# Performance work log

Hardware: AMD Instinct MI355X
Metric: run time of the kernel (lower is better)

Reference implementation:

```python
import jax, jax.numpy as jnp
import numpy as np

B, R, F = 64, 196, 2048   # batch, regions, feature_dim
E, H, A = 512, 512, 512   # embed_dim, hidden_dim, attn_dim
V, L = 12000, 24          # vocab, seq_len


def setup_inputs() -> dict:
    key = jax.random.key(0)
    ks = jax.random.split(key, 16)
    s = lambda *d: 1.0 / np.sqrt(d[-1])
    inp = {
        'image_feats': jax.random.normal(ks[0], (B, R, F), jnp.float32),
        'caption_in': jax.random.randint(ks[1], (B, L), 0, V, jnp.int64),
        'emb_table': jax.random.normal(ks[2], (V, E), jnp.float32) * 0.02,
        'W_init_h': jax.random.normal(ks[3], (H, F), jnp.float32) * s(F),
        'b_init_h': jnp.zeros((H,), jnp.float32),
        'W_init_c': jax.random.normal(ks[4], (H, F), jnp.float32) * s(F),
        'b_init_c': jnp.zeros((H,), jnp.float32),
        'W_ih': jax.random.normal(ks[5], (4 * H, E + F), jnp.float32) * s(E + F),
        'b_ih': jnp.zeros((4 * H,), jnp.float32),
        'W_hh': jax.random.normal(ks[6], (4 * H, H), jnp.float32) * s(H),
        'b_hh': jnp.zeros((4 * H,), jnp.float32),
        'W_featp': jax.random.normal(ks[7], (A, F), jnp.float32) * s(F),
        'b_featp': jnp.zeros((A,), jnp.float32),
        'W_hidp': jax.random.normal(ks[8], (A, H), jnp.float32) * s(H),
        'b_hidp': jnp.zeros((A,), jnp.float32),
        'W_score': jax.random.normal(ks[9], (1, A), jnp.float32) * s(A),
        'b_score': jnp.zeros((1,), jnp.float32),
        'W_out': jax.random.normal(ks[10], (V, H), jnp.float32) * s(H),
        'b_out': jnp.zeros((V,), jnp.float32),
    }
    return inp


def _forward(image_feats, caption_in, emb_table, W_init_h, b_init_h, W_init_c,
             b_init_c, W_ih, b_ih, W_hh, b_hh, W_featp, b_featp, W_hidp,
             b_hidp, W_score, b_score, W_out, b_out):
    # init hidden state from mean image features
    mean_feats = image_feats.mean(axis=1)                      # (B, F)
    h0 = mean_feats @ W_init_h.T + b_init_h                    # (B, H)
    c0 = mean_feats @ W_init_c.T + b_init_c                    # (B, H)

    embeddings = emb_table[caption_in]                         # (B, L, E)  (dropout in eval mode = identity)

    # feature projection is constant over timesteps -> hoist out of the scan
    feat_proj = jnp.einsum('brf,af->bra', image_feats, W_featp) + b_featp  # (B, R, A)

    def step(carry, emb_t):
        h, c = carry
        # additive attention
        hid_proj = h @ W_hidp.T + b_hidp                       # (B, A)
        energy = jnp.tanh(feat_proj + hid_proj[:, None, :])    # (B, R, A)
        scores = jnp.einsum('bra,a->br', energy, W_score[0]) + b_score[0]
        alpha = jax.nn.softmax(scores, axis=1)                 # (B, R)
        context = jnp.einsum('br,brf->bf', alpha, image_feats) # (B, F)
        # LSTM cell (PyTorch gate order: i, f, g, o)
        x = jnp.concatenate([emb_t, context], axis=1)          # (B, E+F)
        gates = x @ W_ih.T + b_ih + h @ W_hh.T + b_hh          # (B, 4H)
        i, f, g, o = jnp.split(gates, 4, axis=1)
        c_new = jax.nn.sigmoid(f) * c + jax.nn.sigmoid(i) * jnp.tanh(g)
        h_new = jax.nn.sigmoid(o) * jnp.tanh(c_new)
        out = h_new @ W_out.T + b_out                          # (B, V)
        return (h_new, c_new), (out, alpha)

    emb_t = jnp.swapaxes(embeddings, 0, 1)                     # (L, B, E)
    _, (preds, alphas) = jax.lax.scan(step, (h0, c0), emb_t)
    predictions = jnp.swapaxes(preds, 0, 1)                    # (B, L, V)
    all_alphas = jnp.swapaxes(alphas, 0, 1)                    # (B, L, R)
    return predictions, all_alphas


def reference(image_feats, caption_in, emb_table, W_init_h, b_init_h, W_init_c,
              b_init_c, W_ih, b_ih, W_hh, b_hh, W_featp, b_featp, W_hidp,
              b_hidp, W_score, b_score, W_out, b_out):
    return _forward(image_feats, caption_in, emb_table, W_init_h, b_init_h,
                    W_init_c, b_init_c, W_ih, b_ih, W_hh, b_hh, W_featp,
                    b_featp, W_hidp, b_hidp, W_score, b_score, W_out, b_out)
```

## Files before the change

kernel.cpp:

```cpp
#include <hip/hip_runtime.h>

#define B_ 64
#define R_ 196
#define F_ 2048
#define E_ 512
#define H_ 512
#define A_ 512
#define V_ 12000
#define L_ 24

typedef __attribute__((ext_vector_type(8))) short bf16x8;
typedef __attribute__((ext_vector_type(8))) unsigned short ushort8_t;
typedef __attribute__((ext_vector_type(4))) float f32x4;
typedef unsigned short ush;

__device__ __forceinline__ float fast_tanh(float x) {
    float t = __expf(2.f * x);
    return 1.f - 2.f / (t + 1.f);
}
__device__ __forceinline__ float fast_sig(float x) {
    return 1.f / (1.f + __expf(-x));
}
__device__ __forceinline__ ush f2bf(float x) {
    unsigned int u = __float_as_uint(x);
    return (ush)((u + 0x7fffu + ((u >> 16) & 1u)) >> 16);
}
__device__ __forceinline__ float bf2f(ush b) {
    return __uint_as_float(((unsigned int)b) << 16);
}

#define LROW 40

template<int SPLIT, int CMAP, bool NFAST>
__global__ __launch_bounds__(256) void gemm_big(
    const ush* __restrict__ Ah, const ush* __restrict__ Al, int lda,
    const ush* __restrict__ Wh, const ush* __restrict__ Wl, int ldw,
    const float* __restrict__ bias, void* __restrict__ Cv,
    int ldc, int N, int K)
{
    constexpr int SMEM_BYTES = (SPLIT == 3) ? 51200 : 25600;
    __shared__ __align__(16) char smem[SMEM_BYTES];
    ush* sAh = (ush*)smem;
    ush* sBh = (ush*)(smem + 5120);
    ush* sAl = (ush*)(smem + 25600);
    ush* sBl = (ush*)(smem + 30720);

    const int tid = threadIdx.x;
    const int lane = tid & 63, w = tid >> 6;

    const int nbx = gridDim.x, nby = gridDim.y;
    const int nwg = nbx * nby;
    int lin = blockIdx.x + nbx * blockIdx.y;
    if ((nwg & 7) == 0) {
        const int q = nwg >> 3;
        lin = (lin & 7) * q + (lin >> 3);
    }
    int bx, by;
    if constexpr (NFAST) { by = lin % nby; bx = lin / nby; }
    else                 { bx = lin % nbx; by = lin / nbx; }
    const int mtile = bx * 64;
    const int ntile = by * 256;

    const int fr = lane & 15, kg = (lane >> 4) * 8;
    const int arow = tid >> 2, aq = (tid & 3) * 8;

    f32x4 acc[4][4];
    #pragma unroll
    for (int mf = 0; mf < 4; ++mf)
        #pragma unroll
        for (int nf = 0; nf < 4; ++nf) acc[mf][nf] = {0.f, 0.f, 0.f, 0.f};

    const uint4 zv = make_uint4(0u, 0u, 0u, 0u);

    for (int kb = 0; kb < K; kb += 32) {
        uint4 a_h = *(const uint4*)(Ah + (size_t)(mtile + arow) * lda + kb + aq);
        uint4 a_l;
        uint4 b_h[4], b_l[4];
        #pragma unroll
        for (int p = 0; p < 4; ++p) {
            const int row = ntile + arow + 64 * p;
            b_h[p] = (row < N) ? *(const uint4*)(Wh + (size_t)row * ldw + kb + aq) : zv;
        }
        if constexpr (SPLIT == 3) {
            a_l = *(const uint4*)(Al + (size_t)(mtile + arow) * lda + kb + aq);
            #pragma unroll
            for (int p = 0; p < 4; ++p) {
                const int row = ntile + arow + 64 * p;
                b_l[p] = (row < N) ? *(const uint4*)(Wl + (size_t)row * ldw + kb + aq) : zv;
            }
        }

        __syncthreads();
        *(uint4*)(sAh + arow * LROW + aq) = a_h;
        #pragma unroll
        for (int p = 0; p < 4; ++p)
            *(uint4*)(sBh + (arow + 64 * p) * LROW + aq) = b_h[p];
        if constexpr (SPLIT == 3) {
            *(uint4*)(sAl + arow * LROW + aq) = a_l;
            #pragma unroll
            for (int p = 0; p < 4; ++p)
                *(uint4*)(sBl + (arow + 64 * p) * LROW + aq) = b_l[p];
        }
        __syncthreads();

        bf16x8 bh[4], bl[4];
        #pragma unroll
        for (int nf = 0; nf < 4; ++nf) {
            bh[nf] = *(const bf16x8*)(sBh + (w * 64 + nf * 16 + fr) * LROW + kg);
            if constexpr (SPLIT == 3)
                bl[nf] = *(const bf16x8*)(sBl + (w * 64 + nf * 16 + fr) * LROW + kg);
        }
        #pragma unroll
        for (int mf = 0; mf < 4; ++mf) {
            const bf16x8 ah = *(const bf16x8*)(sAh + (mf * 16 + fr) * LROW + kg);
            if constexpr (SPLIT == 3) {
                const bf16x8 al = *(const bf16x8*)(sAl + (mf * 16 + fr) * LROW + kg);
                #pragma unroll
                for (int nf = 0; nf < 4; ++nf) {
                    acc[mf][nf] = __builtin_amdgcn_mfma_f32_16x16x32_bf16(ah, bh[nf], acc[mf][nf], 0, 0, 0);
                    acc[mf][nf] = __builtin_amdgcn_mfma_f32_16x16x32_bf16(ah, bl[nf], acc[mf][nf], 0, 0, 0);
                    acc[mf][nf] = __builtin_amdgcn_mfma_f32_16x16x32_bf16(al, bh[nf], acc[mf][nf], 0, 0, 0);
                }
            } else {
                #pragma unroll
                for (int nf = 0; nf < 4; ++nf)
                    acc[mf][nf] = __builtin_amdgcn_mfma_f32_16x16x32_bf16(ah, bh[nf], acc[mf][nf], 0, 0, 0);
            }
        }
    }

    #pragma unroll
    for (int nf = 0; nf < 4; ++nf) {
        const int nn = ntile + w * 64 + nf * 16 + fr;
        if (nn < N) {
            const float bv = bias ? bias[nn] : 0.f;
            #pragma unroll
            for (int mf = 0; mf < 4; ++mf) {
                #pragma unroll
                for (int r = 0; r < 4; ++r) {
                    const int m = mtile + mf * 16 + (lane >> 4) * 4 + r;
                    const float v = acc[mf][nf][r] + bv;
                    if constexpr (CMAP == 1)
                        ((ush*)Cv)[(size_t)m * ldc + nn] = f2bf(v);
                    else if constexpr (CMAP == 2) {
                        float* dst = (float*)Cv + (size_t)(m & 63) * (L_ * V_)
                                   + (size_t)(m >> 6) * V_ + nn;
                        __builtin_nontemporal_store(v, dst);
                    } else
                        ((float*)Cv)[(size_t)m * ldc + nn] = v;
                }
            }
        }
    }
}

__global__ __launch_bounds__(256) void gemm_gates(
    const ush* __restrict__ Ah0, const ush* __restrict__ Al0, int lda0, int k0,
    const ush* __restrict__ Ah1, const ush* __restrict__ Al1, int lda1,
    const ush* __restrict__ Wh, const ush* __restrict__ Wl, int ldw,
    float* __restrict__ C, int ldc, long zstride, int kChunk)
{
    __shared__ ush sAh[64 * LROW];
    __shared__ ush sBh[64 * LROW];
    __shared__ ush sAl[64 * LROW];
    __shared__ ush sBl[64 * LROW];

    const int tid = threadIdx.x;
    const int ntile = blockIdx.x * 64;
    const int kStart = blockIdx.z * kChunk;
    const int lane = tid & 63, w = tid >> 6;
    const int lrow = tid >> 2;
    const int lcol = (tid & 3) * 8;
    const int nrow = ntile + lrow;

    f32x4 acc[4];
    #pragma unroll
    for (int f = 0; f < 4; ++f) acc[f] = {0.f, 0.f, 0.f, 0.f};

    const int fr = lane & 15;
    const int kg = (lane >> 4) * 8;

    for (int kb = kStart; kb < kStart + kChunk; kb += 32) {
        const ush *ph, *pl; int lda, loc;
        if (kb < k0) { ph = Ah0; pl = Al0; lda = lda0; loc = kb; }
        else         { ph = Ah1; pl = Al1; lda = lda1; loc = kb - k0; }

        uint4 a_h = *(const uint4*)(ph + (size_t)lrow * lda + loc + lcol);
        uint4 b_h = *(const uint4*)(Wh + (size_t)nrow * ldw + kb + lcol);
        uint4 a_l = *(const uint4*)(pl + (size_t)lrow * lda + loc + lcol);
        uint4 b_l = *(const uint4*)(Wl + (size_t)nrow * ldw + kb + lcol);

        __syncthreads();
        *(uint4*)(sAh + lrow * LROW + lcol) = a_h;
        *(uint4*)(sBh + lrow * LROW + lcol) = b_h;
        *(uint4*)(sAl + lrow * LROW + lcol) = a_l;
        *(uint4*)(sBl + lrow * LROW + lcol) = b_l;
        __syncthreads();

        const bf16x8 bh = *(const bf16x8*)(sBh + (16 * w + fr) * LROW + kg);
        const bf16x8 bl = *(const bf16x8*)(sBl + (16 * w + fr) * LROW + kg);

        #pragma unroll
        for (int f = 0; f < 4; ++f) {
            const bf16x8 ah = *(const bf16x8*)(sAh + (16 * f + fr) * LROW + kg);
            const bf16x8 al = *(const bf16x8*)(sAl + (16 * f + fr) * LROW + kg);
            acc[f] = __builtin_amdgcn_mfma_f32_16x16x32_bf16(ah, bh, acc[f], 0, 0, 0);
            acc[f] = __builtin_amdgcn_mfma_f32_16x16x32_bf16(ah, bl, acc[f], 0, 0, 0);
            acc[f] = __builtin_amdgcn_mfma_f32_16x16x32_bf16(al, bh, acc[f], 0, 0, 0);
        }
    }

    const int n = ntile + 16 * w + (lane & 15);
    float* Cz = C + (size_t)blockIdx.z * zstride;
    #pragma unroll
    for (int f = 0; f < 4; ++f)
        #pragma unroll
        for (int r = 0; r < 4; ++r) {
            const int m = 16 * f + (lane >> 4) * 4 + r;
            Cz[(size_t)m * ldc + n] = acc[f][r];
        }
}

__global__ __launch_bounds__(256) void prep_feats(
    const float* __restrict__ feats, ush* __restrict__ fbh,
    ush* __restrict__ mh, ush* __restrict__ ml)
{
    const int fs = blockIdx.x;
    const int b  = blockIdx.y;
    const int f = fs * 512 + threadIdx.x * 2;
    const float2* fp = (const float2*)(feats + (size_t)b * R_ * F_ + f);
    ush* fo = fbh + (size_t)b * R_ * F_ + f;
    float sx = 0.f, sy = 0.f;
    for (int r = 0; r < R_; ++r) {
        const float2 v = fp[(size_t)r * (F_ / 2)];
        sx += v.x; sy += v.y;
        ushort2 u; u.x = f2bf(v.x); u.y = f2bf(v.y);
        *(ushort2*)(fo + (size_t)r * F_) = u;
    }
    const float s = 1.f / (float)R_;
    sx *= s; sy *= s;
    const size_t mi = (size_t)b * F_ + f;
    const ush hx = f2bf(sx); mh[mi] = hx;     ml[mi] = f2bf(sx - bf2f(hx));
    const ush hy = f2bf(sy); mh[mi + 1] = hy; ml[mi + 1] = f2bf(sy - bf2f(hy));
}

__global__ __launch_bounds__(256) void gather_split(
    const float* __restrict__ emb, const int* __restrict__ cap,
    ush* __restrict__ eh, ush* __restrict__ el)
{
    const int idx = blockIdx.x * 256 + threadIdx.x;
    const int bt = idx >> 7, j = idx & 127;
    const int tok = cap[bt];
    const float4 v = reinterpret_cast<const float4*>(emb)[(size_t)tok * (E_ / 4) + j];
    const float a[4] = {v.x, v.y, v.z, v.w};
    #pragma unroll
    for (int c = 0; c < 4; ++c) {
        const ush hi = f2bf(a[c]);
        eh[idx * 4 + c] = hi;
        el[idx * 4 + c] = f2bf(a[c] - bf2f(hi));
    }
}

__global__ __launch_bounds__(256) void split_kernel(
    const float* __restrict__ in, ush* __restrict__ hi, ush* __restrict__ lo, int n4)
{
    for (int i = blockIdx.x * 256 + threadIdx.x; i < n4; i += gridDim.x * 256) {
        const float4 v = reinterpret_cast<const float4*>(in)[i];
        const float a[4] = {v.x, v.y, v.z, v.w};
        #pragma unroll
        for (int c = 0; c < 4; ++c) {
            const ush h = f2bf(a[c]);
            hi[i * 4 + c] = h;
            if (lo) lo[i * 4 + c] = f2bf(a[c] - bf2f(h));
        }
    }
}

__global__ __launch_bounds__(256) void prep_wih(
    const float* __restrict__ W_ih, const float* __restrict__ W_hh,
    ush* __restrict__ wxh, ush* __restrict__ wxl,
    ush* __restrict__ wg2h, ush* __restrict__ wg2l)
{
    const int nrow = blockIdx.x;
    for (int k = threadIdx.x; k < E_; k += 256) {
        const float v = W_ih[(size_t)nrow * (E_ + F_) + k];
        const ush h = f2bf(v);
        wxh[(size_t)nrow * E_ + k] = h;
        wxl[(size_t)nrow * E_ + k] = f2bf(v - bf2f(h));
    }
    for (int k = threadIdx.x; k < F_ + H_; k += 256) {
        const float v = (k < F_) ? W_ih[(size_t)nrow * (E_ + F_) + E_ + k]
                                 : W_hh[(size_t)nrow * H_ + (k - F_)];
        const ush h = f2bf(v);
        wg2h[(size_t)nrow * (F_ + H_) + k] = h;
        wg2l[(size_t)nrow * (F_ + H_) + k] = f2bf(v - bf2f(h));
    }
}

__global__ __launch_bounds__(256) void transpose512(
    const float* __restrict__ in, float* __restrict__ out)
{
    const int idx = blockIdx.x * 256 + threadIdx.x;
    const int k = idx >> 9, a = idx & 511;
    out[idx] = in[(size_t)a * 512 + k];
    (void)k;
}

__global__ __launch_bounds__(256) void init_reduce(
    const float* __restrict__ initp, const float* __restrict__ b_init_h,
    const float* __restrict__ b_init_c, float* __restrict__ h0f,
    float* __restrict__ c, ush* __restrict__ h_hi, ush* __restrict__ h_lo)
{
    const int idx = blockIdx.x * 256 + threadIdx.x;
    const int b = idx >> 10, n = idx & 1023;
    float s = 0.f;
    #pragma unroll
    for (int z = 0; z < 8; ++z)
        s += initp[(size_t)z * (B_ * 1024) + (size_t)b * 1024 + n];
    if (n < 512) {
        s += b_init_h[n];
        h0f[b * H_ + n] = s;
        const ush hi = f2bf(s);
        h_hi[b * H_ + n] = hi;
        h_lo[b * H_ + n] = f2bf(s - bf2f(hi));
    } else {
        s += b_init_c[n - 512];
        c[b * H_ + (n - 512)] = s;
    }
}

template<bool ATT>
__global__ __launch_bounds__(512) void step_kernel(
    const float* __restrict__ gparts, const float* __restrict__ egates,
    const float* __restrict__ b_ih, const float* __restrict__ b_hh,
    float* __restrict__ c, const float* __restrict__ h0f,
    ush* __restrict__ h_hi, ush* __restrict__ h_lo,
    ush* __restrict__ hall_hi, ush* __restrict__ hall_lo,
    const float* __restrict__ whpT, const float* __restrict__ b_hidp,
    const ush* __restrict__ fpb, const float* __restrict__ W_score,
    const float* __restrict__ b_score,
    float* __restrict__ alpha, float* __restrict__ alph_out, int t)
{
    __shared__ float sh_h[H_];
    __shared__ float sh_hp[A_];
    __shared__ float sh_ws[A_];
    __shared__ float sh_sc[200];
    __shared__ float red[2];
    const int tid = threadIdx.x;
    const int b = blockIdx.x;
    const int n = tid;

    float hh;
    if (t > 0) {
        const float* eg = egates + ((size_t)b * L_ + (t - 1)) * 2048;
        float gi = b_ih[n] + b_hh[n] + eg[n];
        float gf = b_ih[n + 512] + b_hh[n + 512] + eg[n + 512];
        float gg = b_ih[n + 1024] + b_hh[n + 1024] + eg[n + 1024];
        float go = b_ih[n + 1536] + b_hh[n + 1536] + eg[n + 1536];
        #pragma unroll
        for (int z = 0; z < 8; ++z) {
            const float* gz = gparts + (size_t)z * B_ * 2048 + (size_t)b * 2048;
            gi += gz[n]; gf += gz[n + 512]; gg += gz[n + 1024]; go += gz[n + 1536];
        }
        const float cc = fast_sig(gf) * c[b * H_ + n] + fast_sig(gi) * fast_tanh(gg);
        hh = fast_sig(go) * fast_tanh(cc);
        c[b * H_ + n] = cc;
        const ush hi = f2bf(hh);
        const ush lo = f2bf(hh - bf2f(hi));
        h_hi[b * H_ + n] = hi;
        h_lo[b * H_ + n] = lo;
        const size_t hidx = ((size_t)(t - 1) * B_ + b) * H_ + n;
        hall_hi[hidx] = hi;
        hall_lo[hidx] = lo;
    } else {
        hh = h0f[b * H_ + n];
    }
    if constexpr (!ATT) return;

    sh_h[n] = hh;
    sh_ws[n] = W_score[n];
    __syncthreads();

    {
        float a0 = 0.f, a1 = 0.f, a2 = 0.f, a3 = 0.f;
        #pragma unroll 4
        for (int k = 0; k < H_; k += 4) {
            a0 = fmaf(sh_h[k + 0], whpT[(size_t)(k + 0) * A_ + tid], a0);
            a1 = fmaf(sh_h[k + 1], whpT[(size_t)(k + 1) * A_ + tid], a1);
            a2 = fmaf(sh_h[k + 2], whpT[(size_t)(k + 2) * A_ + tid], a2);
            a3 = fmaf(sh_h[k + 3], whpT[(size_t)(k + 3) * A_ + tid], a3);
        }
        sh_hp[tid] = (a0 + a1) + (a2 + a3) + b_hidp[tid];
    }
    __syncthreads();

    const int lane = tid & 63, wid = tid >> 6;
    for (int r = wid; r < R_; r += 8) {
        const ushort2* row = reinterpret_cast<const ushort2*>(fpb + ((size_t)b * R_ + r) * A_);
        float acc = 0.f;
        #pragma unroll
        for (int j = 0; j < 4; ++j) {
            const ushort2 u = row[lane + 64 * j];
            const int a = 2 * (lane + 64 * j);
            acc += fast_tanh(bf2f(u.x) + sh_hp[a]) * sh_ws[a];
            acc += fast_tanh(bf2f(u.y) + sh_hp[a + 1]) * sh_ws[a + 1];
        }
        for (int off = 32; off > 0; off >>= 1) acc += __shfl_down(acc, off);
        if (lane == 0) sh_sc[r] = acc + b_score[0];
    }
    __syncthreads();

    if (tid < 64) {
        float m = -1e30f;
        for (int r = tid; r < R_; r += 64) m = fmaxf(m, sh_sc[r]);
        for (int off = 32; off > 0; off >>= 1) m = fmaxf(m, __shfl_xor(m, off));
        float s = 0.f;
        for (int r = tid; r < R_; r += 64) s += __expf(sh_sc[r] - m);
        for (int off = 32; off > 0; off >>= 1) s += __shfl_xor(s, off);
        if (tid == 0) { red[0] = m; red[1] = 1.f / s; }
    }
    __syncthreads();
    const float m = red[0], is = red[1];
    if (tid < R_) {
        const float av = __expf(sh_sc[tid] - m) * is;
        alpha[b * R_ + tid] = av;
        alph_out[((size_t)b * L_ + t) * R_ + tid] = av;
    }
}

__global__ __launch_bounds__(256) void ctx_part(
    const ush* __restrict__ fbh, const float* __restrict__ alpha,
    float* __restrict__ ctxp)
{
    __shared__ float sa[28];
    const int rs = blockIdx.x;
    const int b  = blockIdx.y;
    const int tid = threadIdx.x;
    if (tid < 28) sa[tid] = alpha[b * R_ + rs * 28 + tid];
    __syncthreads();

    const int f0 = tid * 8;
    float acc[8] = {0.f, 0.f, 0.f, 0.f, 0.f, 0.f, 0.f, 0.f};
    const ush* base = fbh + ((size_t)b * R_ + rs * 28) * F_ + f0;
    #pragma unroll 4
    for (int i = 0; i < 28; ++i) {
        const ushort8_t u = *(const ushort8_t*)(base + (size_t)i * F_);
        const float a = sa[i];
        #pragma unroll
        for (int j = 0; j < 8; ++j) acc[j] = fmaf(a, bf2f(u[j]), acc[j]);
    }
    float* out = ctxp + ((size_t)(rs * B_ + b)) * F_ + f0;
    *(float4*)(out)     = make_float4(acc[0], acc[1], acc[2], acc[3]);
    *(float4*)(out + 4) = make_float4(acc[4], acc[5], acc[6], acc[7]);
}

__global__ __launch_bounds__(256) void ctx_reduce(
    const float* __restrict__ ctxp, ush* __restrict__ ctx_hi, ush* __restrict__ ctx_lo)
{
    const int idx = blockIdx.x * 256 + threadIdx.x;
    const int b = idx >> 11, f = idx & 2047;
    float s = 0.f;
    #pragma unroll
    for (int rs = 0; rs < 7; ++rs)
        s += ctxp[((size_t)(rs * B_ + b)) * F_ + f];
    const ush hi = f2bf(s);
    ctx_hi[(size_t)b * F_ + f] = hi;
    ctx_lo[(size_t)b * F_ + f] = f2bf(s - bf2f(hi));
}

extern "C" void kernel_launch(void* const* d_in, const int* in_sizes, int n_in,
                              void* d_out, int out_size, void* d_ws, size_t ws_size,
                              hipStream_t stream)
{
    const float* feats    = (const float*)d_in[0];
    const int*   cap      = (const int*)  d_in[1];
    const float* emb      = (const float*)d_in[2];
    const float* W_init_h = (const float*)d_in[3];
    const float* b_init_h = (const float*)d_in[4];
    const float* W_init_c = (const float*)d_in[5];
    const float* b_init_c = (const float*)d_in[6];
    const float* W_ih     = (const float*)d_in[7];
    const float* b_ih     = (const float*)d_in[8];
    const float* W_hh     = (const float*)d_in[9];
    const float* b_hh     = (const float*)d_in[10];
    const float* W_featp  = (const float*)d_in[11];
    const float* b_featp  = (const float*)d_in[12];
    const float* W_hidp   = (const float*)d_in[13];
    const float* b_hidp   = (const float*)d_in[14];
    const float* W_score  = (const float*)d_in[15];
    const float* b_score  = (const float*)d_in[16];
    const float* W_out    = (const float*)d_in[17];
    const float* b_out    = (const float*)d_in[18];

    float* pred     = (float*)d_out;
    float* alph_out = pred + (size_t)B_ * L_ * V_;

    char* p = (char*)d_ws;
    auto alloc = [&](size_t bytes) { char* q = p; p += (bytes + 255) & ~(size_t)255; return q; };

    ush*   fpb    = (ush*)  alloc((size_t)B_ * R_ * A_ * 2);
    ush*   eh     = (ush*)  alloc((size_t)B_ * L_ * E_ * 2);
    ush*   el     = (ush*)  alloc((size_t)B_ * L_ * E_ * 2);
    ush*   mh     = (ush*)  alloc((size_t)B_ * F_ * 2);
    ush*   ml     = (ush*)  alloc((size_t)B_ * F_ * 2);
    ush*   fbh    = (ush*)  alloc((size_t)B_ * R_ * F_ * 2);
    ush*   wfp_h  = (ush*)  alloc((size_t)A_ * F_ * 2);
    ush*   wiH    = (ush*)  alloc((size_t)1024 * F_ * 2);
    ush*   wiL    = (ush*)  alloc((size_t)1024 * F_ * 2);
    ush*   wxh    = (ush*)  alloc((size_t)2048 * E_ * 2);
    ush*   wxl    = (ush*)  alloc((size_t)2048 * E_ * 2);
    ush*   wg2h   = (ush*)  alloc((size_t)2048 * (F_ + H_) * 2);
    ush*   wg2l   = (ush*)  alloc((size_t)2048 * (F_ + H_) * 2);
    ush*   woh    = (ush*)  alloc((size_t)V_ * H_ * 2);
    ush*   wol    = (ush*)  alloc((size_t)V_ * H_ * 2);
    float* whpT   = (float*)alloc((size_t)H_ * A_ * 4);
    float* egates = (float*)alloc((size_t)B_ * L_ * 2048 * 4);
    float* h0f    = (float*)alloc((size_t)B_ * H_ * 4);
    float* c      = (float*)alloc((size_t)B_ * H_ * 4);
    ush*   h_hi   = (ush*)  alloc((size_t)B_ * H_ * 2);
    ush*   h_lo   = (ush*)  alloc((size_t)B_ * H_ * 2);
    ush*   hallh  = (ush*)  alloc((size_t)L_ * B_ * H_ * 2);
    ush*   halll  = (ush*)  alloc((size_t)L_ * B_ * H_ * 2);
    ush*   ctx_hi = (ush*)  alloc((size_t)B_ * F_ * 2);
    ush*   ctx_lo = (ush*)  alloc((size_t)B_ * F_ * 2);
    float* alpha  = (float*)alloc((size_t)B_ * R_ * 4);
    float* gparts = (float*)alloc((size_t)8 * B_ * 2048 * 4);
    float* initp  = (float*)alloc((size_t)8 * B_ * 1024 * 4);
    float* ctxp   = (float*)alloc((size_t)7 * B_ * F_ * 4);

    prep_feats<<<dim3(4, B_), 256, 0, stream>>>(feats, fbh, mh, ml);
    gather_split<<<768, 256, 0, stream>>>(emb, cap, eh, el);
    split_kernel<<<2048, 256, 0, stream>>>(W_out, woh, wol, V_ * H_ / 4);
    split_kernel<<<512, 256, 0, stream>>>(W_init_h, wiH, wiL, H_ * F_ / 4);
    split_kernel<<<512, 256, 0, stream>>>(W_init_c, wiH + (size_t)512 * F_,
                                          wiL + (size_t)512 * F_, H_ * F_ / 4);
    split_kernel<<<512, 256, 0, stream>>>(W_featp, wfp_h, nullptr, A_ * F_ / 4);
    prep_wih<<<2048, 256, 0, stream>>>(W_ih, W_hh, wxh, wxl, wg2h, wg2l);
    transpose512<<<1024, 256, 0, stream>>>(W_hidp, whpT);

    gemm_gates<<<dim3(16, 1, 8), 256, 0, stream>>>(
        mh, ml, F_, F_,
        mh, ml, F_,
        wiH, wiL, F_,
        initp, 1024, (long)B_ * 1024, F_ / 8);
    init_reduce<<<256, 256, 0, stream>>>(initp, b_init_h, b_init_c, h0f, c, h_hi, h_lo);

    gemm_big<1, 1, true><<<dim3(196, 2), 256, 0, stream>>>(
        fbh, nullptr, F_, wfp_h, nullptr, F_, b_featp, fpb, A_, A_, F_);

    gemm_big<3, 0, false><<<dim3(24, 8), 256, 0, stream>>>(
        eh, el, E_, wxh, wxl, E_, nullptr, egates, 2048, 2048, E_);

    for (int t = 0; t < L_; ++t) {
        step_kernel<true><<<B_, 512, 0, stream>>>(
            gparts, egates, b_ih, b_hh, c, h0f, h_hi, h_lo, hallh, halll,
            whpT, b_hidp, fpb, W_score, b_score, alpha, alph_out, t);

        ctx_part<<<dim3(7, B_), 256, 0, stream>>>(fbh, alpha, ctxp);
        ctx_reduce<<<512, 256, 0, stream>>>(ctxp, ctx_hi, ctx_lo);

        gemm_gates<<<dim3(32, 1, 8), 256, 0, stream>>>(
            ctx_hi, ctx_lo, F_, F_,
            h_hi, h_lo, H_,
            wg2h, wg2l, F_ + H_,
            gparts, 4 * H_, (long)B_ * 4 * H_, (F_ + H_) / 8);
    }

    step_kernel<false><<<B_, 512, 0, stream>>>(
        gparts, egates, b_ih, b_hh, c, h0f, h_hi, h_lo, hallh, halll,
        whpT, b_hidp, fpb, W_score, b_score, alpha, alph_out, L_);

    gemm_big<3, 2, false><<<dim3(24, 47), 256, 0, stream>>>(
        hallh, halll, H_, woh, wol, H_, b_out, pred, 0, V_, H_);
}
```

Before: 1.974 ms.

## Use 128x256 GEMM tiles for big GEMMs and fuse context reduction

Adds a 512-thread GEMM variant with 128-row M tiles, so each block covers twice the M extent and W tiles are reused across more rows. It is used for the feature projection and the output vocabulary projection. The per-step context computation is also merged into one kernel that loops over all 196 regions per block, removing the partial-sum buffer and the separate reduce launch. The trade-offs are fewer blocks, more shared memory per block, and a longer serial loop with only 2-element loads per thread in the context kernel.

```diff
diff --git a/kernel.cpp b/kernel.cpp
--- a/kernel.cpp
+++ b/kernel.cpp
@@ -10,7 +10,6 @@
 #define L_ 24
 
 typedef __attribute__((ext_vector_type(8))) short bf16x8;
-typedef __attribute__((ext_vector_type(8))) unsigned short ushort8_t;
 typedef __attribute__((ext_vector_type(4))) float f32x4;
 typedef unsigned short ush;
 
@@ -30,6 +29,129 @@
 }
 
 #define LROW 40
+
+template<int SPLIT, int CMAP, bool NFAST>
+__global__ __launch_bounds__(512) void gemm_big128(
+    const ush* __restrict__ Ah, const ush* __restrict__ Al, int lda,
+    const ush* __restrict__ Wh, const ush* __restrict__ Wl, int ldw,
+    const float* __restrict__ bias, void* __restrict__ Cv,
+    int ldc, int N, int K)
+{
+    constexpr int SMEM_BYTES = (SPLIT == 3) ? 61440 : 30720;
+    __shared__ __align__(16) char smem[SMEM_BYTES];
+    ush* sAh = (ush*)smem;
+    ush* sBh = (ush*)(smem + 10240);
+    ush* sAl = (ush*)(smem + 30720);
+    ush* sBl = (ush*)(smem + 40960);
+
+    const int tid = threadIdx.x;
+    const int lane = tid & 63, w = tid >> 6;
+    const int mw = w >> 2, nw = w & 3;
+
+    const int nbx = gridDim.x, nby = gridDim.y;
+    const int nwg = nbx * nby;
+    const int orig = blockIdx.x + nbx * blockIdx.y;
+    const int q = nwg >> 3, r = nwg & 7;
+    const int xcd = orig & 7, idx = orig >> 3;
+    const int lin = (xcd < r ? xcd * (q + 1) : r * (q + 1) + (xcd - r) * q) + idx;
+    int bx, by;
+    if constexpr (NFAST) { by = lin % nby; bx = lin / nby; }
+    else                 { bx = lin % nbx; by = lin / nbx; }
+    const int mtile = bx * 128;
+    const int ntile = by * 256;
+
+    const int fr = lane & 15, kg = (lane >> 4) * 8;
+    const int arow = tid >> 2, aq = (tid & 3) * 8;
+
+    f32x4 acc[4][4];
+    #pragma unroll
+    for (int mf = 0; mf < 4; ++mf)
+        #pragma unroll
+        for (int nf = 0; nf < 4; ++nf) acc[mf][nf] = {0.f, 0.f, 0.f, 0.f};
+
+    const uint4 zv = make_uint4(0u, 0u, 0u, 0u);
+
+    for (int kb = 0; kb < K; kb += 32) {
+        uint4 a_h = *(const uint4*)(Ah + (size_t)(mtile + arow) * lda + kb + aq);
+        uint4 a_l;
+        uint4 b_h[2], b_l[2];
+        #pragma unroll
+        for (int p = 0; p < 2; ++p) {
+            const int row = ntile + arow + 128 * p;
+            b_h[p] = (row < N) ? *(const uint4*)(Wh + (size_t)row * ldw + kb + aq) : zv;
+        }
+        if constexpr (SPLIT == 3) {
+            a_l = *(const uint4*)(Al + (size_t)(mtile + arow) * lda + kb + aq);
+            #pragma unroll
+            for (int p = 0; p < 2; ++p) {
+                const int row = ntile + arow + 128 * p;
+                b_l[p] = (row < N) ? *(const uint4*)(Wl + (size_t)row * ldw + kb + aq) : zv;
+            }
+        }
+
+        __syncthreads();
+        *(uint4*)(sAh + arow * LROW + aq) = a_h;
+        #pragma unroll
+        for (int p = 0; p < 2; ++p)
+            *(uint4*)(sBh + (arow + 128 * p) * LROW + aq) = b_h[p];
+        if constexpr (SPLIT == 3) {
+            *(uint4*)(sAl + arow * LROW + aq) = a_l;
+            #pragma unroll
+            for (int p = 0; p < 2; ++p)
+                *(uint4*)(sBl + (arow + 128 * p) * LROW + aq) = b_l[p];
+        }
+        __syncthreads();
+
+        bf16x8 bh[4], bl[4];
+        #pragma unroll
+        for (int nf = 0; nf < 4; ++nf) {
+            bh[nf] = *(const bf16x8*)(sBh + (nw * 64 + nf * 16 + fr) * LROW + kg);
+            if constexpr (SPLIT == 3)
+                bl[nf] = *(const bf16x8*)(sBl + (nw * 64 + nf * 16 + fr) * LROW + kg);
+        }
+        #pragma unroll
+        for (int mf = 0; mf < 4; ++mf) {
+            const bf16x8 ah = *(const bf16x8*)(sAh + (mw * 64 + mf * 16 + fr) * LROW + kg);
+            if constexpr (SPLIT == 3) {
+                const bf16x8 al = *(const bf16x8*)(sAl + (mw * 64 + mf * 16 + fr) * LROW + kg);
+                #pragma unroll
+                for (int nf = 0; nf < 4; ++nf) {
+                    acc[mf][nf] = __builtin_amdgcn_mfma_f32_16x16x32_bf16(ah, bh[nf], acc[mf][nf], 0, 0, 0);
+                    acc[mf][nf] = __builtin_amdgcn_mfma_f32_16x16x32_bf16(ah, bl[nf], acc[mf][nf], 0, 0, 0);
+                    acc[mf][nf] = __builtin_amdgcn_mfma_f32_16x16x32_bf16(al, bh[nf], acc[mf][nf], 0, 0, 0);
+                }
+            } else {
+                #pragma unroll
+                for (int nf = 0; nf < 4; ++nf)
+                    acc[mf][nf] = __builtin_amdgcn_mfma_f32_16x16x32_bf16(ah, bh[nf], acc[mf][nf], 0, 0, 0);
+            }
+        }
+    }
+
+    #pragma unroll
+    for (int nf = 0; nf < 4; ++nf) {
+        const int nn = ntile + nw * 64 + nf * 16 + fr;
+        if (nn < N) {
+            const float bv = bias ? bias[nn] : 0.f;
+            #pragma unroll
+            for (int mf = 0; mf < 4; ++mf) {
+                #pragma unroll
+                for (int rr = 0; rr < 4; ++rr) {
+                    const int m = mtile + mw * 64 + mf * 16 + (lane >> 4) * 4 + rr;
+                    const float v = acc[mf][nf][rr] + bv;
+                    if constexpr (CMAP == 1)
+                        ((ush*)Cv)[(size_t)m * ldc + nn] = f2bf(v);
+                    else if constexpr (CMAP == 2) {
+                        float* dst = (float*)Cv + (size_t)(m & 63) * (L_ * V_)
+                                   + (size_t)(m >> 6) * V_ + nn;
+                        __builtin_nontemporal_store(v, dst);
+                    } else
+                        ((float*)Cv)[(size_t)m * ldc + nn] = v;
+                }
+            }
+        }
+    }
+}
 
 template<int SPLIT, int CMAP, bool NFAST>
 __global__ __launch_bounds__(256) void gemm_big(
@@ -137,16 +259,12 @@
             #pragma unroll
             for (int mf = 0; mf < 4; ++mf) {
                 #pragma unroll
-                for (int r = 0; r < 4; ++r) {
-                    const int m = mtile + mf * 16 + (lane >> 4) * 4 + r;
-                    const float v = acc[mf][nf][r] + bv;
+                for (int rr = 0; rr < 4; ++rr) {
+                    const int m = mtile + mf * 16 + (lane >> 4) * 4 + rr;
+                    const float v = acc[mf][nf][rr] + bv;
                     if constexpr (CMAP == 1)
                         ((ush*)Cv)[(size_t)m * ldc + nn] = f2bf(v);
-                    else if constexpr (CMAP == 2) {
-                        float* dst = (float*)Cv + (size_t)(m & 63) * (L_ * V_)
-                                   + (size_t)(m >> 6) * V_ + nn;
-                        __builtin_nontemporal_store(v, dst);
-                    } else
+                    else
                         ((float*)Cv)[(size_t)m * ldc + nn] = v;
                 }
             }
@@ -215,9 +333,9 @@
     #pragma unroll
     for (int f = 0; f < 4; ++f)
         #pragma unroll
-        for (int r = 0; r < 4; ++r) {
-            const int m = 16 * f + (lane >> 4) * 4 + r;
-            Cz[(size_t)m * ldc + n] = acc[f][r];
+        for (int rr = 0; rr < 4; ++rr) {
+            const int m = 16 * f + (lane >> 4) * 4 + rr;
+            Cz[(size_t)m * ldc + n] = acc[f][rr];
         }
 }
 
@@ -428,44 +546,31 @@
     }
 }
 
-__global__ __launch_bounds__(256) void ctx_part(
+__global__ __launch_bounds__(256) void ctx_kernel(
     const ush* __restrict__ fbh, const float* __restrict__ alpha,
-    float* __restrict__ ctxp)
-{
-    __shared__ float sa[28];
-    const int rs = blockIdx.x;
-    const int b  = blockIdx.y;
+    ush* __restrict__ ctx_hi, ush* __restrict__ ctx_lo)
+{
+    __shared__ float sa[R_];
     const int tid = threadIdx.x;
-    if (tid < 28) sa[tid] = alpha[b * R_ + rs * 28 + tid];
+    const int fs = blockIdx.x;
+    const int b = blockIdx.y;
+    if (tid < R_) sa[tid] = alpha[b * R_ + tid];
     __syncthreads();
 
-    const int f0 = tid * 8;
-    float acc[8] = {0.f, 0.f, 0.f, 0.f, 0.f, 0.f, 0.f, 0.f};
-    const ush* base = fbh + ((size_t)b * R_ + rs * 28) * F_ + f0;
+    const int f0 = fs * 512 + tid * 2;
+    const ush* fp = fbh + (size_t)b * R_ * F_ + f0;
+    float cx = 0.f, cy = 0.f;
     #pragma unroll 4
-    for (int i = 0; i < 28; ++i) {
-        const ushort8_t u = *(const ushort8_t*)(base + (size_t)i * F_);
-        const float a = sa[i];
-        #pragma unroll
-        for (int j = 0; j < 8; ++j) acc[j] = fmaf(a, bf2f(u[j]), acc[j]);
-    }
-    float* out = ctxp + ((size_t)(rs * B_ + b)) * F_ + f0;
-    *(float4*)(out)     = make_float4(acc[0], acc[1], acc[2], acc[3]);
-    *(float4*)(out + 4) = make_float4(acc[4], acc[5], acc[6], acc[7]);
-}
-
-__global__ __launch_bounds__(256) void ctx_reduce(
-    const float* __restrict__ ctxp, ush* __restrict__ ctx_hi, ush* __restrict__ ctx_lo)
-{
-    const int idx = blockIdx.x * 256 + threadIdx.x;
-    const int b = idx >> 11, f = idx & 2047;
-    float s = 0.f;
-    #pragma unroll
-    for (int rs = 0; rs < 7; ++rs)
-        s += ctxp[((size_t)(rs * B_ + b)) * F_ + f];
-    const ush hi = f2bf(s);
-    ctx_hi[(size_t)b * F_ + f] = hi;
-    ctx_lo[(size_t)b * F_ + f] = f2bf(s - bf2f(hi));
+    for (int r = 0; r < R_; ++r) {
+        const float a = sa[r];
+        const ushort2 u = *(const ushort2*)(fp + (size_t)r * F_);
+        cx = fmaf(a, bf2f(u.x), cx); cy = fmaf(a, bf2f(u.y), cy);
+    }
+    const size_t ci = (size_t)b * F_ + f0;
+    const ush hx = f2bf(cx);
+    ctx_hi[ci] = hx; ctx_lo[ci] = f2bf(cx - bf2f(hx));
+    const ush hy = f2bf(cy);
+    ctx_hi[ci + 1] = hy; ctx_lo[ci + 1] = f2bf(cy - bf2f(hy));
 }
 
 extern "C" void kernel_launch(void* const* d_in, const int* in_sizes, int n_in,
@@ -526,7 +631,6 @@
     float* alpha  = (float*)alloc((size_t)B_ * R_ * 4);
     float* gparts = (float*)alloc((size_t)8 * B_ * 2048 * 4);
     float* initp  = (float*)alloc((size_t)8 * B_ * 1024 * 4);
-    float* ctxp   = (float*)alloc((size_t)7 * B_ * F_ * 4);
 
     prep_feats<<<dim3(4, B_), 256, 0, stream>>>(feats, fbh, mh, ml);
     gather_split<<<768, 256, 0, stream>>>(emb, cap, eh, el);
@@ -545,7 +649,7 @@
         initp, 1024, (long)B_ * 1024, F_ / 8);
     init_reduce<<<256, 256, 0, stream>>>(initp, b_init_h, b_init_c, h0f, c, h_hi, h_lo);
 
-    gemm_big<1, 1, true><<<dim3(196, 2), 256, 0, stream>>>(
+    gemm_big128<1, 1, true><<<dim3(98, 2), 512, 0, stream>>>(
         fbh, nullptr, F_, wfp_h, nullptr, F_, b_featp, fpb, A_, A_, F_);
 
     gemm_big<3, 0, false><<<dim3(24, 8), 256, 0, stream>>>(
@@ -556,8 +660,7 @@
             gparts, egates, b_ih, b_hh, c, h0f, h_hi, h_lo, hallh, halll,
             whpT, b_hidp, fpb, W_score, b_score, alpha, alph_out, t);
 
-        ctx_part<<<dim3(7, B_), 256, 0, stream>>>(fbh, alpha, ctxp);
-        ctx_reduce<<<512, 256, 0, stream>>>(ctxp, ctx_hi, ctx_lo);
+        ctx_kernel<<<dim3(4, B_), 256, 0, stream>>>(fbh, alpha, ctx_hi, ctx_lo);
 
         gemm_gates<<<dim3(32, 1, 8), 256, 0, stream>>>(
             ctx_hi, ctx_lo, F_, F_,
@@ -570,6 +673,6 @@
         gparts, egates, b_ih, b_hh, c, h0f, h_hi, h_lo, hallh, halll,
         whpT, b_hidp, fpb, W_score, b_score, alpha, alph_out, L_);
 
-    gemm_big<3, 2, false><<<dim3(24, 47), 256, 0, stream>>>(
+    gemm_big128<3, 2, false><<<dim3(12, 47), 512, 0, stream>>>(
         hallh, halll, H_, woh, wol, H_, b_out, pred, 0, V_, H_);
 }
```

New measurement: 2.046 ms. 1.04x slower.
